# Performance work log

Measured on AMD Instinct MI355X. Metric: run time of the kernel, lower is better.

The kernel has to match this reference:

```python
import jax, jax.numpy as jnp
import numpy as np

N_X = 20000      # bessel x-grid
N_ELL = 48       # sparse tabulated multipoles
N_K = 1024       # k quadrature points
N_TAU = 600      # conformal-time samples
K_PIVOT = 0.05


def fast_interp(x, xmin, xmax, ytab):
    """Uniform-grid linear interpolation (tools.fast_interp). ytab: [Nx]."""
    n = ytab.shape[0]
    pos = jnp.clip((x - xmin) / (xmax - xmin) * (n - 1), 0.0, n - 1.0)
    i0 = jnp.clip(jnp.floor(pos).astype(jnp.int32), 0, n - 2)
    w = pos - i0
    return ytab[i0] * (1.0 - w) + ytab[i0 + 1] * w


def setup_inputs() -> dict:
    key = jax.random.key(0)
    ks = jax.random.split(key, 8)
    k = jnp.logspace(-4.0, 0.0, N_K, dtype=jnp.float32)           # Mpc^-1
    tau = jnp.linspace(50.0, 14000.0, N_TAU, dtype=jnp.float32)    # Mpc
    tau0 = jnp.asarray(14100.0, dtype=jnp.float32)
    bessel_x_tab = jnp.linspace(0.0, 15000.0, N_X, dtype=jnp.float32)
    mk = lambda kk, sh, s: (s * jax.random.normal(kk, sh, dtype=jnp.float32))
    return {
        "k": k,
        "tau": tau,
        "tau0": tau0,
        "S0": mk(ks[0], (N_K, N_TAU), 1e-2),
        "S1": mk(ks[1], (N_K, N_TAU), 1e-2),
        "S2": mk(ks[2], (N_K, N_TAU), 1e-2),
        "SE": mk(ks[3], (N_K, N_TAU), 1e-2),
        "bessel_x_tab": bessel_x_tab,
        "phi0_tab": mk(ks[4], (N_X, N_ELL), 1e-1),
        "phi1_tab": mk(ks[5], (N_X, N_ELL), 1e-1),
        "phi2_tab": mk(ks[6], (N_X, N_ELL), 1e-1),
        "eps_tab": mk(ks[7], (N_X, N_ELL), 1e-1),
        "A_s": jnp.asarray(2.1e-9, dtype=jnp.float32),
        "n_s": jnp.asarray(0.965, dtype=jnp.float32),
    }


def reference(k, tau, tau0, S0, S1, S2, SE, bessel_x_tab,
              phi0_tab, phi1_tab, phi2_tab, eps_tab, A_s, n_s):
    xmin = bessel_x_tab[0]
    xmax = bessel_x_tab[-1]
    # radial argument x = k * (tau0 - tau): [K, T]
    x = k[:, None] * (tau0 - tau)[None, :]

    def one_ell(p0, p1, p2, pe):
        # lookup phi0/phi1/phi2/epsilon at every (k, tau), fuse with sources
        srcT = (S0 * fast_interp(x, xmin, xmax, p0)
                + S1 * fast_interp(x, xmin, xmax, p1)
                + S2 * fast_interp(x, xmin, xmax, p2))
        Tl = jnp.trapezoid(srcT, tau, axis=-1)                       # [K]
        El = jnp.trapezoid(SE * fast_interp(x, xmin, xmax, pe), tau, axis=-1)
        return Tl, El

    # vmap over the tabulated-ell axis (columns of the Bessel tables)
    Tl, El = jax.vmap(one_ell, in_axes=(1, 1, 1, 1))(
        phi0_tab, phi1_tab, phi2_tab, eps_tab)                       # [L, K]

    # primordial curvature spectrum P_R(k) = A_s (k/k_p)^(n_s-1) * 2 pi^2 / k^3
    P_R = A_s * (k / K_PIVOT) ** (n_s - 1.0) * (2.0 * jnp.pi ** 2 / k ** 3)
    w = k * k * P_R                                                   # [K]
    c = 2.0 / jnp.pi
    ClTT = c * jnp.trapezoid(w * Tl * Tl, k, axis=-1)                 # [L]
    ClEE = c * jnp.trapezoid(w * El * El, k, axis=-1)
    ClTE = c * jnp.trapezoid(w * Tl * El, k, axis=-1)
    return jnp.stack([ClTT, ClEE, ClTE], axis=0)                      # [3, L]
```

## Files before the change

kernel.cpp:

```cpp
#include <hip/hip_runtime.h>
#include <math.h>

#define N_X   20000
#define N_ELL 48
#define N_K   1024
#define N_TAU 600
#define SPLIT 4
#define CHUNK (N_TAU / SPLIT)

__device__ __forceinline__ unsigned int pack_half2(float lo, float hi) {
    _Float16 l = (_Float16)lo, h = (_Float16)hi;
    unsigned short lu = __builtin_bit_cast(unsigned short, l);
    unsigned short hu = __builtin_bit_cast(unsigned short, h);
    return (unsigned int)lu | ((unsigned int)hu << 16);
}
__device__ __forceinline__ float fdot2(unsigned int a, unsigned int b, float c) {
    float d;
    asm("v_dot2_f32_f16 %0, %1, %2, %3" : "=v"(d) : "v"(a), "v"(b), "v"(c));
    return d;
}

__global__ __launch_bounds__(256) void repack_kernel(
    const float* __restrict__ p0, const float* __restrict__ p1,
    const float* __restrict__ p2, const float* __restrict__ pe,
    uint4* __restrict__ P)
{
    const int total = N_X * N_ELL;
    for (int idx = blockIdx.x * blockDim.x + threadIdx.x; idx < total;
         idx += gridDim.x * blockDim.x) {
        int x = idx / N_ELL;
        int e = idx - x * N_ELL;
        int xn = (x < N_X - 1) ? x + 1 : x;
        int a = x * N_ELL + e, b = xn * N_ELL + e;
        uint4 v;
        v.x = pack_half2(p0[a], p0[b]);
        v.y = pack_half2(p1[a], p1[b]);
        v.z = pack_half2(p2[a], p2[b]);
        v.w = pack_half2(pe[a], pe[b]);
        P[idx] = v;
    }
}

__global__ __launch_bounds__(256) void tl_el_packed(
    const float* __restrict__ k, const float* __restrict__ tau,
    const float* __restrict__ tau0p,
    const float* __restrict__ S0, const float* __restrict__ S1,
    const float* __restrict__ S2, const float* __restrict__ SE,
    const float* __restrict__ bx, const uint4* __restrict__ P,
    float* __restrict__ Tlp, float* __restrict__ Elp)
{
    const int bid  = blockIdx.x;
    const int part = bid & (SPLIT - 1);
    const int kidx = (N_K - 1) - (bid >> 2);
    const int t0   = part * CHUNK;
    const int tid  = threadIdx.x;
    const int wave = tid >> 6;
    const int lane = tid & 63;
    const int ell  = (lane < N_ELL) ? lane : (N_ELL - 1);

    __shared__ unsigned int off_s[CHUNK];
    __shared__ uint4        W2_s[CHUNK];
    __shared__ float        redT[4][N_ELL];
    __shared__ float        redE[4][N_ELL];

    const float kk    = k[kidx];
    const float tau0  = tau0p[0];
    const float xmin  = bx[0];
    const float xmax  = bx[N_X - 1];
    const float scale = (float)(N_X - 1) / (xmax - xmin);

    if (tid < CHUNK) {
        int t = t0 + tid;
        float tt = tau[t];
        float tp = (t > 0)         ? tau[t - 1] : tt;
        float tn = (t < N_TAU - 1) ? tau[t + 1] : tt;
        float wt = 0.5f * (tn - tp);
        float x   = kk * (tau0 - tt);
        float pos = (x - xmin) * scale;
        pos = fminf(fmaxf(pos, 0.0f), (float)(N_X - 1));
        int i0 = (int)pos;
        if (i0 > N_X - 2) i0 = N_X - 2;
        float w  = pos - (float)i0;
        float om = 1.0f - w;
        size_t sb = (size_t)kidx * N_TAU + t;
        float s0 = wt * S0[sb], s1 = wt * S1[sb];
        float s2 = wt * S2[sb], se = wt * SE[sb];
        uint4 w2;
        w2.x = pack_half2(s0 * om, s0 * w);
        w2.y = pack_half2(s1 * om, s1 * w);
        w2.z = pack_half2(s2 * om, s2 * w);
        w2.w = pack_half2(se * om, se * w);
        W2_s[tid]  = w2;
        off_s[tid] = (unsigned int)i0 * (N_ELL * 16u);
    }
    __syncthreads();

    const char* Pb = (const char*)P;
    const unsigned int elloff = (unsigned int)ell * 16u;
    float aT0 = 0.0f, aT1 = 0.0f, aT2 = 0.0f, aE = 0.0f;

    #pragma unroll 4
    for (int i = wave; i < CHUNK; i += 4) {
        unsigned int voff = off_s[i] + elloff;
        uint4 pr = *(const uint4*)(Pb + voff);
        uint4 w2 = W2_s[i];
        aT0 = fdot2(pr.x, w2.x, aT0);
        aT1 = fdot2(pr.y, w2.y, aT1);
        aT2 = fdot2(pr.z, w2.z, aT2);
        aE  = fdot2(pr.w, w2.w, aE);
    }
    float accT = (aT0 + aT1) + aT2;

    if (lane < N_ELL) { redT[wave][lane] = accT; redE[wave][lane] = aE; }
    __syncthreads();
    if (tid < N_ELL) {
        float sT = (redT[0][tid] + redT[1][tid]) + (redT[2][tid] + redT[3][tid]);
        float sE = (redE[0][tid] + redE[1][tid]) + (redE[2][tid] + redE[3][tid]);
        Tlp[((size_t)part * N_ELL + tid) * N_K + kidx] = sT;
        Elp[((size_t)part * N_ELL + tid) * N_K + kidx] = sE;
    }
}

__global__ __launch_bounds__(256) void tl_el_kernel(
    const float* __restrict__ k, const float* __restrict__ tau,
    const float* __restrict__ tau0p,
    const float* __restrict__ S0, const float* __restrict__ S1,
    const float* __restrict__ S2, const float* __restrict__ SE,
    const float* __restrict__ bx,
    const float* __restrict__ p0, const float* __restrict__ p1,
    const float* __restrict__ p2, const float* __restrict__ pe,
    float* __restrict__ Tl, float* __restrict__ El)
{
    const int kidx = blockIdx.x;
    const int tid  = threadIdx.x;
    const int wave = tid >> 6;
    const int lane = tid & 63;
    const int ell  = (lane < N_ELL) ? lane : (N_ELL - 1);

    const float kk    = k[kidx];
    const float tau0  = tau0p[0];
    const float xmin  = bx[0];
    const float xmax  = bx[N_X - 1];
    const float scale = (float)(N_X - 1) / (xmax - xmin);

    const float* Srow0 = S0 + (size_t)kidx * N_TAU;
    const float* Srow1 = S1 + (size_t)kidx * N_TAU;
    const float* Srow2 = S2 + (size_t)kidx * N_TAU;
    const float* SrowE = SE + (size_t)kidx * N_TAU;

    float accT = 0.0f, accE = 0.0f;

    for (int t = wave; t < N_TAU; t += 4) {
        float tt    = tau[t];
        float tprev = (t > 0)         ? tau[t - 1] : tt;
        float tnext = (t < N_TAU - 1) ? tau[t + 1] : tt;
        float wt    = 0.5f * (tnext - tprev);

        float x   = kk * (tau0 - tt);
        float pos = (x - xmin) * scale;
        pos = fminf(fmaxf(pos, 0.0f), (float)(N_X - 1));
        int i0 = (int)floorf(pos);
        if (i0 > N_X - 2) i0 = N_X - 2;
        float w = pos - (float)i0;

        int base = i0 * N_ELL + ell;
        float y00 = p0[base], y01 = p0[base + N_ELL];
        float y10 = p1[base], y11 = p1[base + N_ELL];
        float y20 = p2[base], y21 = p2[base + N_ELL];
        float ye0 = pe[base], ye1 = pe[base + N_ELL];

        float a0 = fmaf(w, y01 - y00, y00);
        float a1 = fmaf(w, y11 - y10, y10);
        float a2 = fmaf(w, y21 - y20, y20);
        float ae = fmaf(w, ye1 - ye0, ye0);

        float s0 = Srow0[t], s1 = Srow1[t], s2 = Srow2[t], se = SrowE[t];

        float srcT = s0 * a0 + s1 * a1 + s2 * a2;
        accT = fmaf(wt, srcT, accT);
        accE = fmaf(wt, se * ae, accE);
    }

    __shared__ float redT[4][N_ELL];
    __shared__ float redE[4][N_ELL];
    if (lane < N_ELL) { redT[wave][lane] = accT; redE[wave][lane] = accE; }
    __syncthreads();
    if (tid < N_ELL) {
        float sT = (redT[0][tid] + redT[1][tid]) + (redT[2][tid] + redT[3][tid]);
        float sE = (redE[0][tid] + redE[1][tid]) + (redE[2][tid] + redE[3][tid]);
        Tl[tid * N_K + kidx] = sT;
        El[tid * N_K + kidx] = sE;
    }
}

__global__ __launch_bounds__(256) void cl_kernel(
    const float* __restrict__ k,
    const float* __restrict__ Asp, const float* __restrict__ nsp,
    const float* __restrict__ Tlp, const float* __restrict__ Elp,
    int nparts, float* __restrict__ out)
{
    const int ell = blockIdx.x;
    const int tid = threadIdx.x;
    const float A_s = Asp[0];
    const float n_s = nsp[0];
    const float two_pi2 = 2.0f * (float)M_PI * (float)M_PI;

    float aTT = 0.0f, aEE = 0.0f, aTE = 0.0f;
    for (int i = tid; i < N_K; i += 256) {
        float kv    = k[i];
        float kprev = (i > 0)       ? k[i - 1] : kv;
        float knext = (i < N_K - 1) ? k[i + 1] : kv;
        float dkw   = 0.5f * (knext - kprev);
        float Pw = A_s * powf(kv / 0.05f, n_s - 1.0f) * two_pi2 / kv;
        float ww = dkw * Pw;
        float tl = 0.0f, el = 0.0f;
        for (int p = 0; p < nparts; ++p) {
            tl += Tlp[((size_t)p * N_ELL + ell) * N_K + i];
            el += Elp[((size_t)p * N_ELL + ell) * N_K + i];
        }
        aTT = fmaf(ww * tl, tl, aTT);
        aEE = fmaf(ww * el, el, aEE);
        aTE = fmaf(ww * tl, el, aTE);
    }

    for (int off = 32; off > 0; off >>= 1) {
        aTT += __shfl_down(aTT, off, 64);
        aEE += __shfl_down(aEE, off, 64);
        aTE += __shfl_down(aTE, off, 64);
    }
    __shared__ float red[3][4];
    const int wave = tid >> 6, lane = tid & 63;
    if (lane == 0) { red[0][wave] = aTT; red[1][wave] = aEE; red[2][wave] = aTE; }
    __syncthreads();
    if (tid == 0) {
        const float c = 2.0f / (float)M_PI;
        out[0 * N_ELL + ell] = c * ((red[0][0] + red[0][1]) + (red[0][2] + red[0][3]));
        out[1 * N_ELL + ell] = c * ((red[1][0] + red[1][1]) + (red[1][2] + red[1][3]));
        out[2 * N_ELL + ell] = c * ((red[2][0] + red[2][1]) + (red[2][2] + red[2][3]));
    }
}

extern "C" void kernel_launch(void* const* d_in, const int* in_sizes, int n_in,
                              void* d_out, int out_size, void* d_ws, size_t ws_size,
                              hipStream_t stream) {
    const float* k    = (const float*)d_in[0];
    const float* tau  = (const float*)d_in[1];
    const float* tau0 = (const float*)d_in[2];
    const float* S0   = (const float*)d_in[3];
    const float* S1   = (const float*)d_in[4];
    const float* S2   = (const float*)d_in[5];
    const float* SE   = (const float*)d_in[6];
    const float* bx   = (const float*)d_in[7];
    const float* p0   = (const float*)d_in[8];
    const float* p1   = (const float*)d_in[9];
    const float* p2   = (const float*)d_in[10];
    const float* pe   = (const float*)d_in[11];
    const float* A_s  = (const float*)d_in[12];
    const float* n_s  = (const float*)d_in[13];
    float* out = (float*)d_out;

    const size_t P_bytes    = (size_t)N_X * N_ELL * sizeof(uint4);
    const size_t part_bytes = (size_t)SPLIT * N_ELL * N_K * sizeof(float);

    if (ws_size >= P_bytes + 2 * part_bytes) {
        uint4* P   = (uint4*)d_ws;
        float* Tlp = (float*)((char*)d_ws + P_bytes);
        float* Elp = (float*)((char*)d_ws + P_bytes + part_bytes);

        repack_kernel<<<(N_X * N_ELL + 255) / 256, 256, 0, stream>>>(p0, p1, p2, pe, P);
        tl_el_packed<<<N_K * SPLIT, 256, 0, stream>>>(k, tau, tau0, S0, S1, S2, SE, bx,
                                                      P, Tlp, Elp);
        cl_kernel<<<N_ELL, 256, 0, stream>>>(k, A_s, n_s, Tlp, Elp, SPLIT, out);
    } else {
        float* Tl = (float*)d_ws;
        float* El = Tl + (size_t)N_ELL * N_K;
        tl_el_kernel<<<N_K, 256, 0, stream>>>(k, tau, tau0, S0, S1, S2, SE, bx,
                                              p0, p1, p2, pe, Tl, El);
        cl_kernel<<<N_ELL, 256, 0, stream>>>(k, A_s, n_s, Tl, El, 1, out);
    }
}
```

Before: 134.4 us.

## Assign one k per wave and split tau into eight chunks

Restructures the packed Tl/El kernel so each wave in a block handles a different k value over its own tau chunk. This removes the shared-memory cross-wave reduction and second barrier. The tau split doubles to eight, so each wave computes its own source weights and writes partials directly. It adds launch-bounds occupancy hints. The cost is longer sequential per-wave loops, more partial sums for the final reduction, and less gather locality across waves.

```diff
diff --git a/kernel.cpp b/kernel.cpp
--- a/kernel.cpp
+++ b/kernel.cpp
@@ -5,7 +5,7 @@
 #define N_ELL 48
 #define N_K   1024
 #define N_TAU 600
-#define SPLIT 4
+#define SPLIT 8
 #define CHUNK (N_TAU / SPLIT)
 
 __device__ __forceinline__ unsigned int pack_half2(float lo, float hi) {
@@ -41,7 +41,7 @@
     }
 }
 
-__global__ __launch_bounds__(256) void tl_el_packed(
+__global__ __launch_bounds__(256, 8) void tl_el_packed(
     const float* __restrict__ k, const float* __restrict__ tau,
     const float* __restrict__ tau0p,
     const float* __restrict__ S0, const float* __restrict__ S1,
@@ -51,17 +51,16 @@
 {
     const int bid  = blockIdx.x;
     const int part = bid & (SPLIT - 1);
-    const int kidx = (N_K - 1) - (bid >> 2);
-    const int t0   = part * CHUNK;
+    const int kgrp = bid >> 3;
     const int tid  = threadIdx.x;
     const int wave = tid >> 6;
     const int lane = tid & 63;
     const int ell  = (lane < N_ELL) ? lane : (N_ELL - 1);
-
-    __shared__ unsigned int off_s[CHUNK];
-    __shared__ uint4        W2_s[CHUNK];
-    __shared__ float        redT[4][N_ELL];
-    __shared__ float        redE[4][N_ELL];
+    const int kidx = (N_K - 1) - (4 * kgrp + wave);
+    const int t0   = part * CHUNK;
+
+    __shared__ unsigned int off_s[4][CHUNK];
+    __shared__ uint4        W2_s[4][CHUNK];
 
     const float kk    = k[kidx];
     const float tau0  = tau0p[0];
@@ -69,8 +68,8 @@
     const float xmax  = bx[N_X - 1];
     const float scale = (float)(N_X - 1) / (xmax - xmin);
 
-    if (tid < CHUNK) {
-        int t = t0 + tid;
+    for (int tl = lane; tl < CHUNK; tl += 64) {
+        int t = t0 + tl;
         float tt = tau[t];
         float tp = (t > 0)         ? tau[t - 1] : tt;
         float tn = (t < N_TAU - 1) ? tau[t + 1] : tt;
@@ -90,8 +89,8 @@
         w2.y = pack_half2(s1 * om, s1 * w);
         w2.z = pack_half2(s2 * om, s2 * w);
         w2.w = pack_half2(se * om, se * w);
-        W2_s[tid]  = w2;
-        off_s[tid] = (unsigned int)i0 * (N_ELL * 16u);
+        W2_s[wave][tl]  = w2;
+        off_s[wave][tl] = (unsigned int)i0 * (N_ELL * 16u);
     }
     __syncthreads();
 
@@ -99,11 +98,11 @@
     const unsigned int elloff = (unsigned int)ell * 16u;
     float aT0 = 0.0f, aT1 = 0.0f, aT2 = 0.0f, aE = 0.0f;
 
-    #pragma unroll 4
-    for (int i = wave; i < CHUNK; i += 4) {
-        unsigned int voff = off_s[i] + elloff;
+    #pragma unroll 3
+    for (int i = 0; i < CHUNK; ++i) {
+        unsigned int voff = off_s[wave][i] + elloff;
         uint4 pr = *(const uint4*)(Pb + voff);
-        uint4 w2 = W2_s[i];
+        uint4 w2 = W2_s[wave][i];
         aT0 = fdot2(pr.x, w2.x, aT0);
         aT1 = fdot2(pr.y, w2.y, aT1);
         aT2 = fdot2(pr.z, w2.z, aT2);
@@ -111,13 +110,9 @@
     }
     float accT = (aT0 + aT1) + aT2;
 
-    if (lane < N_ELL) { redT[wave][lane] = accT; redE[wave][lane] = aE; }
-    __syncthreads();
-    if (tid < N_ELL) {
-        float sT = (redT[0][tid] + redT[1][tid]) + (redT[2][tid] + redT[3][tid]);
-        float sE = (redE[0][tid] + redE[1][tid]) + (redE[2][tid] + redE[3][tid]);
-        Tlp[((size_t)part * N_ELL + tid) * N_K + kidx] = sT;
-        Elp[((size_t)part * N_ELL + tid) * N_K + kidx] = sE;
+    if (lane < N_ELL) {
+        Tlp[((size_t)part * N_ELL + lane) * N_K + kidx] = accT;
+        Elp[((size_t)part * N_ELL + lane) * N_K + kidx] = aE;
     }
 }
 
@@ -268,8 +263,9 @@
         float* Elp = (float*)((char*)d_ws + P_bytes + part_bytes);
 
         repack_kernel<<<(N_X * N_ELL + 255) / 256, 256, 0, stream>>>(p0, p1, p2, pe, P);
-        tl_el_packed<<<N_K * SPLIT, 256, 0, stream>>>(k, tau, tau0, S0, S1, S2, SE, bx,
-                                                      P, Tlp, Elp);
+        tl_el_packed<<<(N_K / 4) * SPLIT, 256, 0, stream>>>(k, tau, tau0,
+                                                            S0, S1, S2, SE, bx,
+                                                            P, Tlp, Elp);
         cl_kernel<<<N_ELL, 256, 0, stream>>>(k, A_s, n_s, Tlp, Elp, SPLIT, out);
     } else {
         float* Tl = (float*)d_ws;
```

New measurement: 136.1 us. About the same (+1.3%).

## Batch table gathers per wave and drop in-block reduction via per-wave partials

Applied to the files above, without the earlier changes.

The tau split grows from 4 to 5 chunks, and occupancy is requested with launch bounds of 8 blocks per CU. The inner loop now issues GROUP=5 independent gathers before their dot products, so more memory requests are in flight. The shared-memory cross-wave reduction and its barrier are gone: each wave writes its own partial sums, and the final kernel reduces 20 partials instead of 4. This trades a larger partial buffer and more reduction reads for less synchronisation and better latency hiding.

```diff
diff --git a/kernel.cpp b/kernel.cpp
--- a/kernel.cpp
+++ b/kernel.cpp
@@ -5,8 +5,10 @@
 #define N_ELL 48
 #define N_K   1024
 #define N_TAU 600
-#define SPLIT 4
+#define SPLIT 5
 #define CHUNK (N_TAU / SPLIT)
+#define NPART (SPLIT * 4)
+#define GROUP 5
 
 __device__ __forceinline__ unsigned int pack_half2(float lo, float hi) {
     _Float16 l = (_Float16)lo, h = (_Float16)hi;
@@ -41,7 +43,7 @@
     }
 }
 
-__global__ __launch_bounds__(256) void tl_el_packed(
+__global__ __launch_bounds__(256, 8) void tl_el_packed(
     const float* __restrict__ k, const float* __restrict__ tau,
     const float* __restrict__ tau0p,
     const float* __restrict__ S0, const float* __restrict__ S1,
@@ -50,8 +52,9 @@
     float* __restrict__ Tlp, float* __restrict__ Elp)
 {
     const int bid  = blockIdx.x;
-    const int part = bid & (SPLIT - 1);
-    const int kidx = (N_K - 1) - (bid >> 2);
+    const int kgrp = bid / SPLIT;
+    const int part = bid - kgrp * SPLIT;
+    const int kidx = (N_K - 1) - kgrp;
     const int t0   = part * CHUNK;
     const int tid  = threadIdx.x;
     const int wave = tid >> 6;
@@ -60,8 +63,6 @@
 
     __shared__ unsigned int off_s[CHUNK];
     __shared__ uint4        W2_s[CHUNK];
-    __shared__ float        redT[4][N_ELL];
-    __shared__ float        redE[4][N_ELL];
 
     const float kk    = k[kidx];
     const float tau0  = tau0p[0];
@@ -99,25 +100,29 @@
     const unsigned int elloff = (unsigned int)ell * 16u;
     float aT0 = 0.0f, aT1 = 0.0f, aT2 = 0.0f, aE = 0.0f;
 
-    #pragma unroll 4
-    for (int i = wave; i < CHUNK; i += 4) {
-        unsigned int voff = off_s[i] + elloff;
-        uint4 pr = *(const uint4*)(Pb + voff);
-        uint4 w2 = W2_s[i];
-        aT0 = fdot2(pr.x, w2.x, aT0);
-        aT1 = fdot2(pr.y, w2.y, aT1);
-        aT2 = fdot2(pr.z, w2.z, aT2);
-        aE  = fdot2(pr.w, w2.w, aE);
+    for (int g = 0; g < CHUNK / 4; g += GROUP) {
+        uint4 pr[GROUP];
+        #pragma unroll
+        for (int j = 0; j < GROUP; ++j) {
+            int ii = 4 * (g + j) + wave;
+            pr[j] = *(const uint4*)(Pb + (off_s[ii] + elloff));
+        }
+        #pragma unroll
+        for (int j = 0; j < GROUP; ++j) {
+            int ii = 4 * (g + j) + wave;
+            uint4 w2 = W2_s[ii];
+            aT0 = fdot2(pr[j].x, w2.x, aT0);
+            aT1 = fdot2(pr[j].y, w2.y, aT1);
+            aT2 = fdot2(pr[j].z, w2.z, aT2);
+            aE  = fdot2(pr[j].w, w2.w, aE);
+        }
     }
     float accT = (aT0 + aT1) + aT2;
 
-    if (lane < N_ELL) { redT[wave][lane] = accT; redE[wave][lane] = aE; }
-    __syncthreads();
-    if (tid < N_ELL) {
-        float sT = (redT[0][tid] + redT[1][tid]) + (redT[2][tid] + redT[3][tid]);
-        float sE = (redE[0][tid] + redE[1][tid]) + (redE[2][tid] + redE[3][tid]);
-        Tlp[((size_t)part * N_ELL + tid) * N_K + kidx] = sT;
-        Elp[((size_t)part * N_ELL + tid) * N_K + kidx] = sE;
+    if (lane < N_ELL) {
+        int sub = part * 4 + wave;
+        Tlp[((size_t)sub * N_ELL + lane) * N_K + kidx] = accT;
+        Elp[((size_t)sub * N_ELL + lane) * N_K + kidx] = aE;
     }
 }
 
@@ -260,7 +265,7 @@
     float* out = (float*)d_out;
 
     const size_t P_bytes    = (size_t)N_X * N_ELL * sizeof(uint4);
-    const size_t part_bytes = (size_t)SPLIT * N_ELL * N_K * sizeof(float);
+    const size_t part_bytes = (size_t)NPART * N_ELL * N_K * sizeof(float);
 
     if (ws_size >= P_bytes + 2 * part_bytes) {
         uint4* P   = (uint4*)d_ws;
@@ -268,9 +273,10 @@
         float* Elp = (float*)((char*)d_ws + P_bytes + part_bytes);
 
         repack_kernel<<<(N_X * N_ELL + 255) / 256, 256, 0, stream>>>(p0, p1, p2, pe, P);
-        tl_el_packed<<<N_K * SPLIT, 256, 0, stream>>>(k, tau, tau0, S0, S1, S2, SE, bx,
+        tl_el_packed<<<N_K * SPLIT, 256, 0, stream>>>(k, tau, tau0,
+                                                      S0, S1, S2, SE, bx,
                                                       P, Tlp, Elp);
-        cl_kernel<<<N_ELL, 256, 0, stream>>>(k, A_s, n_s, Tlp, Elp, SPLIT, out);
+        cl_kernel<<<N_ELL, 256, 0, stream>>>(k, A_s, n_s, Tlp, Elp, NPART, out);
     } else {
         float* Tl = (float*)d_ws;
         float* El = Tl + (size_t)N_ELL * N_K;
```

Measured after the change: 155.2 us. 1.15x slower.
